# Kernel tuning notes

Measured on AMD Instinct MI355X. Metric: run time of the kernel, lower is better.

Reference implementation:

```python
import jax, jax.numpy as jnp
import numpy as np

N = 100000
E = 3200000
IN_DIM, HID, MLP_HID, K = 3, 64, 128, 15


def setup_inputs() -> dict:
    key = jax.random.key(0)
    ks = jax.random.split(key, 10)
    x = jax.random.normal(ks[0], (N, IN_DIM), dtype=jnp.float32)
    edge_index = jax.random.randint(ks[1], (2, E), 0, N, dtype=jnp.int32)
    def glorot(k, shape):
        lim = float(np.sqrt(6.0 / (shape[0] + shape[1])))
        return jax.random.uniform(k, shape, jnp.float32, -lim, lim)
    return {
        "x": x,
        "edge_index": edge_index,
        "W1": glorot(ks[2], (IN_DIM, HID)), "b1": jnp.zeros((HID,), jnp.float32),
        "W2": glorot(ks[3], (HID, HID)),    "b2": jnp.zeros((HID,), jnp.float32),
        "Wm1": glorot(ks[4], (HID, MLP_HID)), "bm1": jnp.zeros((MLP_HID,), jnp.float32),
        "Wm2": glorot(ks[5], (MLP_HID, K)),   "bm2": jnp.zeros((K,), jnp.float32),
    }


def _gcn_layer(h, W, b, src, dst, deg_inv_sqrt, n):
    # h: [N, Fin] -> [N, Fout]; GCNConv: D^-1/2 (A+I) D^-1/2 (h W) + b
    hw = h @ W  # dense GEMM first (Fin small)
    norm = deg_inv_sqrt[src] * deg_inv_sqrt[dst]  # [E+N]
    msg = hw[src] * norm[:, None]                 # irregular gather, [E+N, Fout]
    out = jax.ops.segment_sum(msg, dst, num_segments=n)  # scatter-add
    return out + b


def reference(x, edge_index, W1, b1, W2, b2, Wm1, bm1, Wm2, bm2):
    n = x.shape[0]
    loops = jnp.arange(n, dtype=edge_index.dtype)
    src = jnp.concatenate([edge_index[0], loops])  # self-loops appended
    dst = jnp.concatenate([edge_index[1], loops])
    deg = jax.ops.segment_sum(jnp.ones_like(dst, dtype=x.dtype), dst, num_segments=n)
    deg_inv_sqrt = jnp.where(deg > 0, jax.lax.rsqrt(jnp.maximum(deg, 1.0)), 0.0)

    h = jax.nn.elu(_gcn_layer(x, W1, b1, src, dst, deg_inv_sqrt, n))
    h = jax.nn.elu(_gcn_layer(h, W2, b2, src, dst, deg_inv_sqrt, n))
    # MLP (dropout is identity in eval mode)
    h = jax.nn.elu(h @ Wm1 + bm1)
    H = h @ Wm2 + bm2
    return jax.nn.softmax(H, axis=1)  # [N, K]
```

## Files before the change

kernel.cpp:

```cpp
#include <hip/hip_runtime.h>
#include <hip/hip_fp16.h>
#include <math.h>


#define SPAN 128
#define CAP  4608
#define CH   8192
#define EPT  16
#define H2P  88
#define MSP2 136

typedef _Float16 v8hf __attribute__((ext_vector_type(8)));
typedef float    v4f  __attribute__((ext_vector_type(4)));

__device__ __forceinline__ float elu(float v) { return v > 0.f ? v : expm1f(v); }

__global__ __launch_bounds__(512) void scatter_kernel(const int* __restrict__ src,
    const int* __restrict__ dst, int* __restrict__ cursor, unsigned* __restrict__ colb,
    const float* __restrict__ W2, const float* __restrict__ Wm1,
    const float* __restrict__ Wm2, __half* __restrict__ W2t,
    __half* __restrict__ Wm1t, __half* __restrict__ Wm2p,
    int E, int NBK, int nChunks) {
    int tid = threadIdx.x;
    if ((int)blockIdx.x == nChunks) {
        for (int i = tid; i < 64 * 64; i += 512) {
            int f = i >> 6, k = i & 63;
            W2t[f * 64 + k] = __float2half(W2[k * 64 + f]);
        }
        for (int i = tid; i < 128 * 64; i += 512) {
            int j = i >> 6, f = i & 63;
            Wm1t[j * 64 + f] = __float2half(Wm1[f * 128 + j]);
        }
        for (int i = tid; i < 4 * 64 * 8; i += 512) {
            int j = i & 7, l = (i >> 3) & 63, t = i >> 9;
            int k = t * 32 + (l >> 4) * 8 + j;
            int c = l & 15;
            Wm2p[i] = (c < 15) ? __float2half(Wm2[k * 15 + c]) : __half(0.f);
        }
        return;
    }
    __shared__ int hist[1024];
    __shared__ unsigned gb[1024];
    int chunk = blockIdx.x;
    for (int i = tid; i < NBK; i += 512) hist[i] = 0;
    __syncthreads();
    int base = chunk * CH;
    int cnt = min(CH, E - base);
    unsigned br[EPT], dt[EPT];
#pragma unroll
    for (int j = 0; j < EPT; ++j) {
        int idx = j * 512 + tid;
        br[j] = 0xFFFFFFFFu;
        if (idx < cnt) {
            int e = base + idx;
            int s = src[e], d = dst[e];
            int b = d >> 7;
            int r = atomicAdd(&hist[b], 1);
            br[j] = ((unsigned)b << 13) | (unsigned)r;
            dt[j] = ((unsigned)(d & 127) << 17) | (unsigned)s;
        }
    }
    __syncthreads();
    for (int b = tid; b < NBK; b += 512) {
        int c = hist[b];
        gb[b] = (unsigned)(b * CAP) + (c ? (unsigned)atomicAdd(&cursor[b], c) : 0u);
    }
    __syncthreads();
#pragma unroll
    for (int j = 0; j < EPT; ++j) {
        if (br[j] != 0xFFFFFFFFu) {
            int b = br[j] >> 13;
            int r = br[j] & 8191;
            unsigned pos = gb[b] + (unsigned)r;
            if (pos < (unsigned)(b + 1) * CAP) colb[pos] = dt[j];
        }
    }
}

__global__ __launch_bounds__(256) void csr_sort_kernel(const unsigned* __restrict__ colb,
    const int* __restrict__ cursor, const float* __restrict__ x,
    int* __restrict__ row_ptr, int* __restrict__ col,
    float* __restrict__ dis, __half* __restrict__ sxh, int N, int NBK) {
    __shared__ unsigned ebuf[CAP];
    __shared__ int sbuf[CAP];
    __shared__ int cnt[SPAN], pref[SPAN], fill[SPAN];
    __shared__ int redbuf[256];
    int b = blockIdx.x, tid = threadIdx.x;
    int n = min(cursor[b], CAP);
    int base = b * CAP;
    int partial = 0;
    for (int i2 = tid; i2 < b; i2 += 256) partial += min(cursor[i2], CAP);
    redbuf[tid] = partial;
    if (tid < SPAN) cnt[tid] = 0;
    for (int i = tid; i < n; i += 256) ebuf[i] = colb[base + i];
    __syncthreads();
    for (int off = 128; off; off >>= 1) {
        if (tid < off) redbuf[tid] += redbuf[tid + off];
        __syncthreads();
    }
    int bb = redbuf[0];
    for (int i = tid; i < n; i += 256) atomicAdd(&cnt[(ebuf[i] >> 17) & 127], 1);
    __syncthreads();
    if (tid < SPAN) pref[tid] = cnt[tid];
    __syncthreads();
    for (int off = 1; off < SPAN; off <<= 1) {
        int xv = (tid < SPAN && tid >= off) ? pref[tid - off] : 0;
        __syncthreads();
        if (tid < SPAN) pref[tid] += xv;
        __syncthreads();
    }
    if (tid < SPAN) {
        int ex = pref[tid] - cnt[tid];
        fill[tid] = ex;
        int node = b * SPAN + tid;
        if (node < N) {
            row_ptr[node] = bb + ex;
            float r = rsqrtf((float)(cnt[tid] + 1));
            dis[node] = r;
            __half2 h0 = __floats2half2_rn(r * x[node * 3 + 0], r * x[node * 3 + 1]);
            __half2 h1 = __floats2half2_rn(r * x[node * 3 + 2], 0.f);
            uint2 w; w.x = *(unsigned*)&h0; w.y = *(unsigned*)&h1;
            *(uint2*)(sxh + (size_t)node * 4) = w;
        }
    }
    if (b == NBK - 1 && tid == 0) row_ptr[N] = bb + n;
    __syncthreads();
    for (int i = tid; i < n; i += 256) {
        unsigned e = ebuf[i];
        int pos = atomicAdd(&fill[(e >> 17) & 127], 1);
        sbuf[pos] = (int)(e & 0x1FFFF);
    }
    __syncthreads();
    for (int i = tid; i < n; i += 256) col[bb + i] = sbuf[i];
}

__global__ void agg3_kernel(const __half* __restrict__ sxh, const int* __restrict__ row_ptr,
                            const int* __restrict__ col, const float* __restrict__ dis,
                            const float* __restrict__ W1, const float* __restrict__ b1,
                            __half* __restrict__ s1h, int N) {
    int wave = (blockIdx.x * blockDim.x + threadIdx.x) >> 6;
    int lane = threadIdx.x & 63;
    if (wave >= N) return;
    int d = wave;
    int start = row_ptr[d], end = row_ptr[d + 1];
    float a0 = 0.f, a1 = 0.f, a2v = 0.f;
    for (int i = start + lane; i < end; i += 64) {
        uint2 rq = *(const uint2*)(sxh + (size_t)col[i] * 4);
        float2 u0 = __half22float2(*(__half2*)&rq.x);
        float2 u1 = __half22float2(*(__half2*)&rq.y);
        a0 += u0.x; a1 += u0.y; a2v += u1.x;
    }
#pragma unroll
    for (int off = 32; off; off >>= 1) {
        a0  += __shfl_xor(a0, off);
        a1  += __shfl_xor(a1, off);
        a2v += __shfl_xor(a2v, off);
    }
    {
        uint2 rq = *(const uint2*)(sxh + (size_t)d * 4);
        float2 u0 = __half22float2(*(__half2*)&rq.x);
        float2 u1 = __half22float2(*(__half2*)&rq.y);
        a0 += u0.x; a1 += u0.y; a2v += u1.x;
    }
    float r = dis[d];
    float v = r * (a0 * W1[lane] + a1 * W1[64 + lane] + a2v * W1[128 + lane]) + b1[lane];
    s1h[(size_t)d * 64 + lane] = __float2half(r * elu(v));
}

__global__ void agg64_kernel(const __half2* __restrict__ s1h, const int* __restrict__ row_ptr,
                             const int* __restrict__ col, const float* __restrict__ dis,
                             __half2* __restrict__ a2h, int N) {
    int wave = (blockIdx.x * blockDim.x + threadIdx.x) >> 6;
    int lane = threadIdx.x & 63;
    int hl = lane & 31;
    int d = wave * 2 + (lane >> 5);
    bool act = d < N;
    int start = 0, end = 0;
    if (act) { start = row_ptr[d]; end = row_ptr[d + 1]; }
    float a0x = 0.f, a0y = 0.f, a1x = 0.f, a1y = 0.f;
    float a2x = 0.f, a2y = 0.f, a3x = 0.f, a3y = 0.f;
    float a4x = 0.f, a4y = 0.f, a5x = 0.f, a5y = 0.f;
    float a6x = 0.f, a6y = 0.f, a7x = 0.f, a7y = 0.f;
    if (act) {
        float2 v = __half22float2(s1h[(size_t)d * 32 + hl]);
        a0x = v.x; a0y = v.y;
    }
    int i = start;
    for (; i + 7 < end; i += 8) {
        int c0 = col[i],     c1 = col[i + 1], c2 = col[i + 2], c3 = col[i + 3];
        int c4 = col[i + 4], c5 = col[i + 5], c6 = col[i + 6], c7 = col[i + 7];
        float2 v0 = __half22float2(s1h[(size_t)c0 * 32 + hl]);
        float2 v1 = __half22float2(s1h[(size_t)c1 * 32 + hl]);
        float2 v2 = __half22float2(s1h[(size_t)c2 * 32 + hl]);
        float2 v3 = __half22float2(s1h[(size_t)c3 * 32 + hl]);
        float2 v4 = __half22float2(s1h[(size_t)c4 * 32 + hl]);
        float2 v5 = __half22float2(s1h[(size_t)c5 * 32 + hl]);
        float2 v6 = __half22float2(s1h[(size_t)c6 * 32 + hl]);
        float2 v7 = __half22float2(s1h[(size_t)c7 * 32 + hl]);
        a0x += v0.x; a0y += v0.y; a1x += v1.x; a1y += v1.y;
        a2x += v2.x; a2y += v2.y; a3x += v3.x; a3y += v3.y;
        a4x += v4.x; a4y += v4.y; a5x += v5.x; a5y += v5.y;
        a6x += v6.x; a6y += v6.y; a7x += v7.x; a7y += v7.y;
    }
    for (; i < end; ++i) {
        float2 v = __half22float2(s1h[(size_t)col[i] * 32 + hl]);
        a0x += v.x; a0y += v.y;
    }
    if (act) {
        float r = dis[d];
        float ox = r * (((a0x + a1x) + (a2x + a3x)) + ((a4x + a5x) + (a6x + a7x)));
        float oy = r * (((a0y + a1y) + (a2y + a3y)) + ((a4y + a5y) + (a6y + a7y)));
        a2h[(size_t)d * 32 + hl] = __floats2half2_rn(ox, oy);
    }
}

__global__ __launch_bounds__(256) void h1_kernel(const __half* __restrict__ a2h,
    const __half* __restrict__ W2t, const float* __restrict__ b2g,
    const __half* __restrict__ Wm1t, const float* __restrict__ bm1g,
    const __half* __restrict__ Wm2p, const float* __restrict__ bm2g,
    float* __restrict__ out, int N) {
    __shared__ __align__(16) __half h2s[64 * H2P];
    __shared__ __align__(16) __half ms[64 * MSP2];
    int tid = threadIdx.x;
    int wave = tid >> 6, lane = tid & 63;
    int q = lane >> 4, l16 = lane & 15;
    int base = blockIdx.x * 64;

    v8hf wc[4];
#pragma unroll
    for (int t = 0; t < 4; ++t)
        wc[t] = *(const v8hf*)(Wm2p + ((size_t)(t * 64 + lane)) * 8);
    float bbc = (l16 < 15) ? bm2g[l16] : 0.f;

    {
        int nodeRow = base + wave * 16 + l16;
        size_t arow = (size_t)min(nodeRow, N - 1) * 64;
        v8hf af0 = *(const v8hf*)(a2h + arow + q * 8);
        v8hf af1 = *(const v8hf*)(a2h + arow + 32 + q * 8);
#pragma unroll
        for (int fb = 0; fb < 4; ++fb) {
            float bb = b2g[fb * 16 + l16];
            v4f acc = {bb, bb, bb, bb};
            v8hf b0 = *(const v8hf*)(W2t + (fb * 16 + l16) * 64 + q * 8);
            v8hf b1 = *(const v8hf*)(W2t + (fb * 16 + l16) * 64 + 32 + q * 8);
            acc = __builtin_amdgcn_mfma_f32_16x16x32_f16(af0, b0, acc, 0, 0, 0);
            acc = __builtin_amdgcn_mfma_f32_16x16x32_f16(af1, b1, acc, 0, 0, 0);
#pragma unroll
            for (int r = 0; r < 4; ++r)
                h2s[(wave * 16 + q * 4 + r) * H2P + fb * 16 + l16] =
                    __float2half(elu(acc[r]));
        }
    }
    __syncthreads();
    {
        int arow = (wave * 16 + l16) * H2P;
        v8hf af0 = *(const v8hf*)(h2s + arow + q * 8);
        v8hf af1 = *(const v8hf*)(h2s + arow + 32 + q * 8);
#pragma unroll
        for (int jb = 0; jb < 8; ++jb) {
            float bb = bm1g[jb * 16 + l16];
            v4f acc = {bb, bb, bb, bb};
            v8hf b0 = *(const v8hf*)(Wm1t + (jb * 16 + l16) * 64 + q * 8);
            v8hf b1 = *(const v8hf*)(Wm1t + (jb * 16 + l16) * 64 + 32 + q * 8);
            acc = __builtin_amdgcn_mfma_f32_16x16x32_f16(af0, b0, acc, 0, 0, 0);
            acc = __builtin_amdgcn_mfma_f32_16x16x32_f16(af1, b1, acc, 0, 0, 0);
#pragma unroll
            for (int r = 0; r < 4; ++r)
                ms[(wave * 16 + q * 4 + r) * MSP2 + jb * 16 + l16] =
                    __float2half(elu(acc[r]));
        }
    }
    __syncthreads();
    {
        int arow = (wave * 16 + l16) * MSP2;
        v4f accC = {bbc, bbc, bbc, bbc};
#pragma unroll
        for (int t = 0; t < 4; ++t) {
            v8hf a = *(const v8hf*)(ms + arow + t * 32 + q * 8);
            accC = __builtin_amdgcn_mfma_f32_16x16x32_f16(a, wc[t], accC, 0, 0, 0);
        }
#pragma unroll
        for (int r = 0; r < 4; ++r) {
            float lg = (l16 < 15) ? accC[r] : -1e30f;
            float mx = lg;
            mx = fmaxf(mx, __shfl_xor(mx, 1));
            mx = fmaxf(mx, __shfl_xor(mx, 2));
            mx = fmaxf(mx, __shfl_xor(mx, 4));
            mx = fmaxf(mx, __shfl_xor(mx, 8));
            float ex = (l16 < 15) ? __expf(lg - mx) : 0.f;
            float sden = ex;
            sden += __shfl_xor(sden, 1);
            sden += __shfl_xor(sden, 2);
            sden += __shfl_xor(sden, 4);
            sden += __shfl_xor(sden, 8);
            int node = base + wave * 16 + q * 4 + r;
            if (l16 < 15 && node < N)
                out[(size_t)node * 15 + l16] = ex / sden;
        }
    }
}

extern "C" void kernel_launch(void* const* d_in, const int* in_sizes, int n_in,
                              void* d_out, int out_size, void* d_ws, size_t ws_size,
                              hipStream_t stream) {
    const float* x   = (const float*)d_in[0];
    const int*   ei  = (const int*)d_in[1];
    const float* W1  = (const float*)d_in[2];
    const float* b1  = (const float*)d_in[3];
    const float* W2  = (const float*)d_in[4];
    const float* b2  = (const float*)d_in[5];
    const float* Wm1 = (const float*)d_in[6];
    const float* bm1 = (const float*)d_in[7];
    const float* Wm2 = (const float*)d_in[8];
    const float* bm2 = (const float*)d_in[9];
    float* out = (float*)d_out;

    int N = in_sizes[0] / 3;
    int E = in_sizes[1] / 2;
    const int* src = ei;
    const int* dst = ei + E;
    int NBK = (N + SPAN - 1) / SPAN;

    uintptr_t p = (uintptr_t)d_ws;
    auto carve = [&](size_t bytes) -> void* {
        p = (p + 255) & ~(uintptr_t)255;
        void* r = (void*)p;
        p += bytes;
        return r;
    };
    __half*   a2h     = (__half*)carve((size_t)N * 64 * 2);
    __half*   s1h     = (__half*)carve((size_t)N * 64 * 2);
    int*      cursor  = (int*)carve((size_t)NBK * 4);
    int*      row_ptr = (int*)carve((size_t)(N + 1) * 4);
    float*    dis     = (float*)carve((size_t)N * 4);
    __half*   sxh     = (__half*)carve((size_t)N * 8);
    int*      col     = (int*)carve((size_t)E * 4);
    __half*   W2t     = (__half*)carve(64 * 64 * 2);
    __half*   Wm1t    = (__half*)carve(128 * 64 * 2);
    __half*   Wm2p    = (__half*)carve(4 * 64 * 8 * 2);
    unsigned* colb = (unsigned*)a2h;

    int nChunks = (E + CH - 1) / CH;
    int waveBlocks3  = (N + 3) / 4;
    int waveBlocks64 = (N + 7) / 8;
    int nTiles = (N + 63) / 64;

    hipMemsetAsync(cursor, 0, (size_t)NBK * 4, stream);
    scatter_kernel<<<nChunks + 1, 512, 0, stream>>>(src, dst, cursor, colb,
        W2, Wm1, Wm2, W2t, Wm1t, Wm2p, E, NBK, nChunks);
    csr_sort_kernel<<<NBK, 256, 0, stream>>>(colb, cursor, x, row_ptr, col, dis, sxh, N, NBK);
    agg3_kernel<<<waveBlocks3, 256, 0, stream>>>(sxh, row_ptr, col, dis, W1, b1, s1h, N);
    agg64_kernel<<<waveBlocks64, 256, 0, stream>>>((const __half2*)s1h, row_ptr, col, dis,
                                                   (__half2*)a2h, N);
    h1_kernel<<<nTiles, 256, 0, stream>>>(a2h, W2t, b2, Wm1t, bm1, Wm2p, bm2, out, N);
}
```

Before: 246.7 us.

## Sort CSR in place within padded buckets and use start/end pairs

The CSR sort now writes sorted columns back into the padded per-bucket buffer and stores per-node (start,end) pairs, so the per-block prefix sum over earlier buckets and the separate compact col array are gone. The sort kernel uses 512 threads with vectorised uint4 copies. agg3 handles two nodes per wave with half-wave lanes, and agg64 pre-adds pairs of fp16 neighbour values before converting to fp32, halving accumulator registers. The costs are a larger workspace for the padded colb buffer and some fp16 precision loss from the pairwise half additions.

After: 243.7 us. No clear change (-1.2%).

```diff
diff --git a/kernel.cpp b/kernel.cpp
--- a/kernel.cpp
+++ b/kernel.cpp
@@ -77,29 +77,23 @@
     }
 }
 
-__global__ __launch_bounds__(256) void csr_sort_kernel(const unsigned* __restrict__ colb,
+__global__ __launch_bounds__(512) void csr_sort_kernel(unsigned* __restrict__ colb,
     const int* __restrict__ cursor, const float* __restrict__ x,
-    int* __restrict__ row_ptr, int* __restrict__ col,
-    float* __restrict__ dis, __half* __restrict__ sxh, int N, int NBK) {
-    __shared__ unsigned ebuf[CAP];
-    __shared__ int sbuf[CAP];
+    uint2* __restrict__ rp2, float* __restrict__ dis, __half* __restrict__ sxh,
+    int N) {
+    __shared__ __align__(16) unsigned ebuf[CAP];
+    __shared__ __align__(16) int sbuf[CAP];
     __shared__ int cnt[SPAN], pref[SPAN], fill[SPAN];
-    __shared__ int redbuf[256];
     int b = blockIdx.x, tid = threadIdx.x;
     int n = min(cursor[b], CAP);
-    int base = b * CAP;
-    int partial = 0;
-    for (int i2 = tid; i2 < b; i2 += 256) partial += min(cursor[i2], CAP);
-    redbuf[tid] = partial;
+    size_t base = (size_t)b * CAP;
     if (tid < SPAN) cnt[tid] = 0;
-    for (int i = tid; i < n; i += 256) ebuf[i] = colb[base + i];
-    __syncthreads();
-    for (int off = 128; off; off >>= 1) {
-        if (tid < off) redbuf[tid] += redbuf[tid + off];
-        __syncthreads();
-    }
-    int bb = redbuf[0];
-    for (int i = tid; i < n; i += 256) atomicAdd(&cnt[(ebuf[i] >> 17) & 127], 1);
+    int n4 = n >> 2;
+    for (int k = tid; k < n4; k += 512)
+        *(uint4*)(ebuf + 4 * k) = *(const uint4*)(colb + base + 4 * k);
+    for (int i = (n4 << 2) + tid; i < n; i += 512) ebuf[i] = colb[base + i];
+    __syncthreads();
+    for (int i = tid; i < n; i += 512) atomicAdd(&cnt[(ebuf[i] >> 17) & 127], 1);
     __syncthreads();
     if (tid < SPAN) pref[tid] = cnt[tid];
     __syncthreads();
@@ -114,7 +108,10 @@
         fill[tid] = ex;
         int node = b * SPAN + tid;
         if (node < N) {
-            row_ptr[node] = bb + ex;
+            uint2 rp;
+            rp.x = (unsigned)(base + ex);
+            rp.y = (unsigned)(base + ex + cnt[tid]);
+            rp2[node] = rp;
             float r = rsqrtf((float)(cnt[tid] + 1));
             dis[node] = r;
             __half2 h0 = __floats2half2_rn(r * x[node * 3 + 0], r * x[node * 3 + 1]);
@@ -123,52 +120,57 @@
             *(uint2*)(sxh + (size_t)node * 4) = w;
         }
     }
-    if (b == NBK - 1 && tid == 0) row_ptr[N] = bb + n;
-    __syncthreads();
-    for (int i = tid; i < n; i += 256) {
+    __syncthreads();
+    for (int i = tid; i < n; i += 512) {
         unsigned e = ebuf[i];
         int pos = atomicAdd(&fill[(e >> 17) & 127], 1);
         sbuf[pos] = (int)(e & 0x1FFFF);
     }
     __syncthreads();
-    for (int i = tid; i < n; i += 256) col[bb + i] = sbuf[i];
-}
-
-__global__ void agg3_kernel(const __half* __restrict__ sxh, const int* __restrict__ row_ptr,
-                            const int* __restrict__ col, const float* __restrict__ dis,
+    for (int k = tid; k < n4; k += 512)
+        *(uint4*)(colb + base + 4 * k) = *(const uint4*)(sbuf + 4 * k);
+    for (int i = (n4 << 2) + tid; i < n; i += 512) colb[base + i] = (unsigned)sbuf[i];
+}
+
+__global__ void agg3_kernel(const __half* __restrict__ sxh, const uint2* __restrict__ rp2,
+                            const unsigned* __restrict__ colb, const float* __restrict__ dis,
                             const float* __restrict__ W1, const float* __restrict__ b1,
                             __half* __restrict__ s1h, int N) {
     int wave = (blockIdx.x * blockDim.x + threadIdx.x) >> 6;
     int lane = threadIdx.x & 63;
-    if (wave >= N) return;
-    int d = wave;
-    int start = row_ptr[d], end = row_ptr[d + 1];
+    int hl = lane & 31;
+    int d = wave * 2 + (lane >> 5);
+    bool act = d < N;
+    int start = 0, end = 0;
+    if (act) { uint2 rp = rp2[d]; start = (int)rp.x; end = (int)rp.y; }
     float a0 = 0.f, a1 = 0.f, a2v = 0.f;
-    for (int i = start + lane; i < end; i += 64) {
-        uint2 rq = *(const uint2*)(sxh + (size_t)col[i] * 4);
+    for (int i = start + hl; i < end; i += 32) {
+        uint2 rq = *(const uint2*)(sxh + (size_t)colb[i] * 4);
         float2 u0 = __half22float2(*(__half2*)&rq.x);
         float2 u1 = __half22float2(*(__half2*)&rq.y);
         a0 += u0.x; a1 += u0.y; a2v += u1.x;
     }
 #pragma unroll
-    for (int off = 32; off; off >>= 1) {
+    for (int off = 16; off; off >>= 1) {
         a0  += __shfl_xor(a0, off);
         a1  += __shfl_xor(a1, off);
         a2v += __shfl_xor(a2v, off);
     }
-    {
+    if (act) {
         uint2 rq = *(const uint2*)(sxh + (size_t)d * 4);
         float2 u0 = __half22float2(*(__half2*)&rq.x);
         float2 u1 = __half22float2(*(__half2*)&rq.y);
         a0 += u0.x; a1 += u0.y; a2v += u1.x;
-    }
-    float r = dis[d];
-    float v = r * (a0 * W1[lane] + a1 * W1[64 + lane] + a2v * W1[128 + lane]) + b1[lane];
-    s1h[(size_t)d * 64 + lane] = __float2half(r * elu(v));
-}
-
-__global__ void agg64_kernel(const __half2* __restrict__ s1h, const int* __restrict__ row_ptr,
-                             const int* __restrict__ col, const float* __restrict__ dis,
+        float r = dis[d];
+        float v0 = r * (a0 * W1[hl]      + a1 * W1[64 + hl]      + a2v * W1[128 + hl])      + b1[hl];
+        float v1 = r * (a0 * W1[32 + hl] + a1 * W1[96 + hl]      + a2v * W1[160 + hl])      + b1[32 + hl];
+        s1h[(size_t)d * 64 + hl]      = __float2half(r * elu(v0));
+        s1h[(size_t)d * 64 + 32 + hl] = __float2half(r * elu(v1));
+    }
+}
+
+__global__ void agg64_kernel(const __half2* __restrict__ s1h, const uint2* __restrict__ rp2,
+                             const unsigned* __restrict__ colb, const float* __restrict__ dis,
                              __half2* __restrict__ a2h, int N) {
     int wave = (blockIdx.x * blockDim.x + threadIdx.x) >> 6;
     int lane = threadIdx.x & 63;
@@ -176,40 +178,42 @@
     int d = wave * 2 + (lane >> 5);
     bool act = d < N;
     int start = 0, end = 0;
-    if (act) { start = row_ptr[d]; end = row_ptr[d + 1]; }
+    if (act) { uint2 rp = rp2[d]; start = (int)rp.x; end = (int)rp.y; }
     float a0x = 0.f, a0y = 0.f, a1x = 0.f, a1y = 0.f;
     float a2x = 0.f, a2y = 0.f, a3x = 0.f, a3y = 0.f;
-    float a4x = 0.f, a4y = 0.f, a5x = 0.f, a5y = 0.f;
-    float a6x = 0.f, a6y = 0.f, a7x = 0.f, a7y = 0.f;
     if (act) {
         float2 v = __half22float2(s1h[(size_t)d * 32 + hl]);
         a0x = v.x; a0y = v.y;
     }
     int i = start;
     for (; i + 7 < end; i += 8) {
-        int c0 = col[i],     c1 = col[i + 1], c2 = col[i + 2], c3 = col[i + 3];
-        int c4 = col[i + 4], c5 = col[i + 5], c6 = col[i + 6], c7 = col[i + 7];
-        float2 v0 = __half22float2(s1h[(size_t)c0 * 32 + hl]);
-        float2 v1 = __half22float2(s1h[(size_t)c1 * 32 + hl]);
-        float2 v2 = __half22float2(s1h[(size_t)c2 * 32 + hl]);
-        float2 v3 = __half22float2(s1h[(size_t)c3 * 32 + hl]);
-        float2 v4 = __half22float2(s1h[(size_t)c4 * 32 + hl]);
-        float2 v5 = __half22float2(s1h[(size_t)c5 * 32 + hl]);
-        float2 v6 = __half22float2(s1h[(size_t)c6 * 32 + hl]);
-        float2 v7 = __half22float2(s1h[(size_t)c7 * 32 + hl]);
-        a0x += v0.x; a0y += v0.y; a1x += v1.x; a1y += v1.y;
-        a2x += v2.x; a2y += v2.y; a3x += v3.x; a3y += v3.y;
-        a4x += v4.x; a4y += v4.y; a5x += v5.x; a5y += v5.y;
-        a6x += v6.x; a6y += v6.y; a7x += v7.x; a7y += v7.y;
+        int c0 = (int)colb[i],     c1 = (int)colb[i + 1];
+        int c2 = (int)colb[i + 2], c3 = (int)colb[i + 3];
+        int c4 = (int)colb[i + 4], c5 = (int)colb[i + 5];
+        int c6 = (int)colb[i + 6], c7 = (int)colb[i + 7];
+        __half2 v0 = s1h[(size_t)c0 * 32 + hl];
+        __half2 v1 = s1h[(size_t)c1 * 32 + hl];
+        __half2 v2 = s1h[(size_t)c2 * 32 + hl];
+        __half2 v3 = s1h[(size_t)c3 * 32 + hl];
+        __half2 v4 = s1h[(size_t)c4 * 32 + hl];
+        __half2 v5 = s1h[(size_t)c5 * 32 + hl];
+        __half2 v6 = s1h[(size_t)c6 * 32 + hl];
+        __half2 v7 = s1h[(size_t)c7 * 32 + hl];
+        float2 p0 = __half22float2(__hadd2(v0, v1));
+        float2 p1 = __half22float2(__hadd2(v2, v3));
+        float2 p2 = __half22float2(__hadd2(v4, v5));
+        float2 p3 = __half22float2(__hadd2(v6, v7));
+        a0x += p0.x; a0y += p0.y; a1x += p1.x; a1y += p1.y;
+        a2x += p2.x; a2y += p2.y; a3x += p3.x; a3y += p3.y;
     }
     for (; i < end; ++i) {
-        float2 v = __half22float2(s1h[(size_t)col[i] * 32 + hl]);
+        float2 v = __half22float2(s1h[(size_t)colb[i] * 32 + hl]);
         a0x += v.x; a0y += v.y;
     }
     if (act) {
         float r = dis[d];
-        float ox = r * (((a0x + a1x) + (a2x + a3x)) + ((a4x + a5x) + (a6x + a7x)));
-        float oy = r * (((a0y + a1y) + (a2y + a3y)) + ((a4y + a5y) + (a6y + a7y)));
+        float ox = r * ((a0x + a1x) + (a2x + a3x));
+        float oy = r * ((a0y + a1y) + (a2y + a3y));
         a2h[(size_t)d * 32 + hl] = __floats2half2_rn(ox, oy);
     }
 }
@@ -328,29 +332,27 @@
         p += bytes;
         return r;
     };
+    unsigned* colb    = (unsigned*)carve((size_t)NBK * CAP * 4);
     __half*   a2h     = (__half*)carve((size_t)N * 64 * 2);
     __half*   s1h     = (__half*)carve((size_t)N * 64 * 2);
     int*      cursor  = (int*)carve((size_t)NBK * 4);
-    int*      row_ptr = (int*)carve((size_t)(N + 1) * 4);
+    uint2*    rp2     = (uint2*)carve((size_t)N * 8);
     float*    dis     = (float*)carve((size_t)N * 4);
     __half*   sxh     = (__half*)carve((size_t)N * 8);
-    int*      col     = (int*)carve((size_t)E * 4);
     __half*   W2t     = (__half*)carve(64 * 64 * 2);
     __half*   Wm1t    = (__half*)carve(128 * 64 * 2);
     __half*   Wm2p    = (__half*)carve(4 * 64 * 8 * 2);
-    unsigned* colb = (unsigned*)a2h;
 
     int nChunks = (E + CH - 1) / CH;
-    int waveBlocks3  = (N + 3) / 4;
-    int waveBlocks64 = (N + 7) / 8;
+    int aggBlocks = (N + 7) / 8;
     int nTiles = (N + 63) / 64;
 
     hipMemsetAsync(cursor, 0, (size_t)NBK * 4, stream);
     scatter_kernel<<<nChunks + 1, 512, 0, stream>>>(src, dst, cursor, colb,
         W2, Wm1, Wm2, W2t, Wm1t, Wm2p, E, NBK, nChunks);
-    csr_sort_kernel<<<NBK, 256, 0, stream>>>(colb, cursor, x, row_ptr, col, dis, sxh, N, NBK);
-    agg3_kernel<<<waveBlocks3, 256, 0, stream>>>(sxh, row_ptr, col, dis, W1, b1, s1h, N);
-    agg64_kernel<<<waveBlocks64, 256, 0, stream>>>((const __half2*)s1h, row_ptr, col, dis,
-                                                   (__half2*)a2h, N);
+    csr_sort_kernel<<<NBK, 512, 0, stream>>>(colb, cursor, x, rp2, dis, sxh, N);
+    agg3_kernel<<<aggBlocks, 256, 0, stream>>>(sxh, rp2, colb, dis, W1, b1, s1h, N);
+    agg64_kernel<<<aggBlocks, 256, 0, stream>>>((const __half2*)s1h, rp2, colb, dis,
+                                                (__half2*)a2h, N);
     h1_kernel<<<nTiles, 256, 0, stream>>>(a2h, W2t, b2, Wm1t, bm1, Wm2p, bm2, out, N);
 }
```
